# Kernel optimization log

Measured on AMD Instinct MI355X. Metric: run time of the kernel, lower is better.

Reference implementation:

```python
import jax, jax.numpy as jnp
import numpy as np

R = 8  # rnn_radius
C = 64  # channels


def _shift(x, dh, dw):
    # out[b, h, w, c] = x[b, h - dh, w - dw, c], zero padded (matches SAME conv with a single masked tap)
    B, H, W, Cc = x.shape
    x = jnp.pad(x, ((0, 0), (max(dh, 0), max(-dh, 0)), (max(dw, 0), max(-dw, 0)), (0, 0)))
    return x[:, max(-dh, 0):max(-dh, 0) + H, max(-dw, 0):max(-dw, 0) + W, :]


def _direction(x, W, dh, dw):
    # recurrent: t = relu(shift(t) @ W); acc = x + sum_t over R steps
    def step(carry, _):
        t, acc = carry
        t = jax.nn.relu(jnp.einsum('bhwc,cd->bhwd', _shift(t, dh, dw), W))
        return (t, acc + t), None
    (_, acc), _ = jax.lax.scan(step, (x, x), None, length=R)
    return acc


def setup_inputs() -> dict:
    key = jax.random.key(0)
    kx, kl, kr, ku, kd = jax.random.split(key, 5)
    x = jax.random.normal(kx, (8, 192, 192, C), dtype=jnp.float32)
    # masked kernels reduce to a single CxC channel-mix matrix per direction
    # (keras 'random_normal' initializer: stddev 0.05)
    W_left = jax.random.normal(kl, (C, C), dtype=jnp.float32) * 0.05
    W_right = jax.random.normal(kr, (C, C), dtype=jnp.float32) * 0.05
    W_up = jax.random.normal(ku, (C, C), dtype=jnp.float32) * 0.05
    W_down = jax.random.normal(kd, (C, C), dtype=jnp.float32) * 0.05
    return {"x": x, "W_left": W_left, "W_right": W_right, "W_up": W_up, "W_down": W_down}


def reference(x, W_left, W_right, W_up, W_down):
    # kernel_switch tap positions: left -> out[w]=in[w-1]; right -> out[w]=in[w+1];
    # up -> out[h]=in[h-1]; down -> out[h]=in[h+1]
    outs = [
        _direction(x, W_left, 0, 1),
        _direction(x, W_right, 0, -1),
        _direction(x, W_up, 1, 0),
        _direction(x, W_down, -1, 0),
    ]
    return jnp.concatenate(outs, axis=3)
```

## Files before the change

kernel.cpp:

```cpp
#include <hip/hip_runtime.h>
#include <hip/hip_bf16.h>


#define HD 192
#define CH 64
#define RSTEPS 8
#define TSTRIDE 72
#define SLOTS 193
#define STG_STRIDE 68

typedef __attribute__((ext_vector_type(8))) short short8v;
typedef __attribute__((ext_vector_type(4))) float float4v;

static __device__ __forceinline__ short f2bf_rne(float f) {
    unsigned u = __float_as_uint(f);
    u += 0x7FFFu + ((u >> 16) & 1u);
    return (short)(u >> 16);
}

__global__ __launch_bounds__(256) void spatial_rnn_kernel(
    const float* __restrict__ x,
    const float* __restrict__ Wl,
    const float* __restrict__ Wr,
    const float* __restrict__ Wu,
    const float* __restrict__ Wd,
    float* __restrict__ out)
{
    __shared__ __align__(16) short smem_s[2 * SLOTS * TSTRIDE];
    short* tb0 = smem_s;
    short* tb1 = smem_s + SLOTS * TSTRIDE;
    float* stg = (float*)smem_s;

    const int tid  = threadIdx.x;
    const int dir  = blockIdx.y;
    const int line = blockIdx.x;
    const int b    = line / HD;
    const int rc   = line - b * HD;

    const float* Wp = (dir == 0) ? Wl : (dir == 1) ? Wr : (dir == 2) ? Wu : Wd;

    int xbase, xstride, obase, ostride;
    if (dir == 0) {
        xbase   = (b * HD + rc) * HD * CH;
        xstride = CH;
        obase   = (b * HD + rc) * HD * 256;
        ostride = 256;
    } else if (dir == 1) {
        xbase   = ((b * HD + rc) * HD + (HD - 1)) * CH;
        xstride = -CH;
        obase   = ((b * HD + rc) * HD + (HD - 1)) * 256 + 64;
        ostride = -256;
    } else if (dir == 2) {
        xbase   = b * HD * HD * CH + rc * CH;
        xstride = HD * CH;
        obase   = b * HD * HD * 256 + rc * 256 + 128;
        ostride = HD * 256;
    } else {
        xbase   = ((b * HD + (HD - 1)) * HD + rc) * CH;
        xstride = -HD * CH;
        obase   = ((b * HD + (HD - 1)) * HD + rc) * 256 + 192;
        ostride = -HD * 256;
    }

    for (int q = tid; q < HD * 16; q += 256) {
        int p  = q >> 4;
        int c4 = (q & 15) << 2;
        const float4 v = *(const float4*)(x + xbase + p * xstride + c4);
        short4 s;
        s.x = f2bf_rne(v.x); s.y = f2bf_rne(v.y);
        s.z = f2bf_rne(v.z); s.w = f2bf_rne(v.w);
        *(short4*)(tb0 + (p + 1) * TSTRIDE + c4) = s;
    }
    if (tid < TSTRIDE) { tb0[tid] = 0; tb1[tid] = 0; }

    const int lane = tid & 63;
    const int wv   = tid >> 6;
    const int q4   = lane >> 4;
    const int l16  = lane & 15;

    short8v Af[2][4];
    #pragma unroll
    for (int kc = 0; kc < 2; ++kc)
        #pragma unroll
        for (int dt = 0; dt < 4; ++dt)
            #pragma unroll
            for (int j = 0; j < 8; ++j)
                Af[kc][dt][j] = f2bf_rne(Wp[(kc * 32 + q4 * 8 + j) * CH + dt * 16 + l16]);

    float4v acc[3][4];
    #pragma unroll
    for (int i = 0; i < 3; ++i)
        #pragma unroll
        for (int dt = 0; dt < 4; ++dt)
            acc[i][dt] = (float4v){0.f, 0.f, 0.f, 0.f};

    __syncthreads();

    for (int k = 0; k < RSTEPS; ++k) {
        const short* cur = (k & 1) ? tb1 : tb0;
        short*       nxt = (k & 1) ? tb0 : tb1;
        #pragma unroll
        for (int i = 0; i < 3; ++i) {
            const int pb   = (wv + i * 4) * 16;
            const int slot = pb + l16;
            short8v B0 = *(const short8v*)(cur + slot * TSTRIDE + q4 * 8);
            short8v B1 = *(const short8v*)(cur + slot * TSTRIDE + 32 + q4 * 8);
            #pragma unroll
            for (int dt = 0; dt < 4; ++dt) {
                float4v d = {0.f, 0.f, 0.f, 0.f};
                d = __builtin_amdgcn_mfma_f32_16x16x32_bf16(Af[0][dt], B0, d, 0, 0, 0);
                d = __builtin_amdgcn_mfma_f32_16x16x32_bf16(Af[1][dt], B1, d, 0, 0, 0);
                float v0 = fmaxf(d[0], 0.f);
                float v1 = fmaxf(d[1], 0.f);
                float v2 = fmaxf(d[2], 0.f);
                float v3 = fmaxf(d[3], 0.f);
                acc[i][dt][0] += v0; acc[i][dt][1] += v1;
                acc[i][dt][2] += v2; acc[i][dt][3] += v3;
                if (k < RSTEPS - 1) {
                    __hip_bfloat162 h01 = __float22bfloat162_rn(make_float2(v0, v1));
                    __hip_bfloat162 h23 = __float22bfloat162_rn(make_float2(v2, v3));
                    uint2 wpk;
                    __builtin_memcpy(&wpk.x, &h01, 4);
                    __builtin_memcpy(&wpk.y, &h23, 4);
                    *(uint2*)(nxt + (pb + l16 + 1) * TSTRIDE + dt * 16 + q4 * 4) = wpk;
                }
            }
        }
        __syncthreads();
    }

    #pragma unroll
    for (int i = 0; i < 3; ++i) {
        const int pb = (wv + i * 4) * 16;
        #pragma unroll
        for (int dt = 0; dt < 4; ++dt) {
            *(float4v*)(stg + (pb + l16) * STG_STRIDE + dt * 16 + q4 * 4) = acc[i][dt];
        }
    }
    __syncthreads();

    for (int q = tid; q < HD * 16; q += 256) {
        int p  = q >> 4;
        int c4 = (q & 15) << 2;
        const float4  xv = *(const float4*)(x + xbase + p * xstride + c4);
        const float4v sv = *(const float4v*)(stg + p * STG_STRIDE + c4);
        float4 o;
        o.x = xv.x + sv[0]; o.y = xv.y + sv[1];
        o.z = xv.z + sv[2]; o.w = xv.w + sv[3];
        *(float4*)(out + obase + p * ostride + c4) = o;
    }
}

extern "C" void kernel_launch(void* const* d_in, const int* in_sizes, int n_in,
                              void* d_out, int out_size, void* d_ws, size_t ws_size,
                              hipStream_t stream) {
    const float* x  = (const float*)d_in[0];
    const float* Wl = (const float*)d_in[1];
    const float* Wr = (const float*)d_in[2];
    const float* Wu = (const float*)d_in[3];
    const float* Wd = (const float*)d_in[4];
    float* outp = (float*)d_out;
    dim3 grid(8 * HD, 4);
    spatial_rnn_kernel<<<grid, 256, 0, stream>>>(x, Wl, Wr, Wu, Wd, outp);
}
```

Measured before the change: 518.7 us.

## Single-buffer LDS state, load x in MFMA layout, drop staging pass

Switches from double-buffered LDS to a single buffer: each step loads its B fragments into registers, syncs, then overwrites the buffer in place. x is now loaded directly in the MFMA output layout, which seeds the accumulator and the bf16 state in one pass. The epilogue writes the accumulators straight to global memory, removing the LDS staging step and the second read of x. Halving LDS use and adding a launch-bounds occupancy hint of 4 blocks should raise occupancy, at the cost of an extra barrier per step and less coalesced global accesses.

```diff
diff --git a/kernel.cpp b/kernel.cpp
--- a/kernel.cpp
+++ b/kernel.cpp
@@ -7,7 +7,6 @@
 #define RSTEPS 8
 #define TSTRIDE 72
 #define SLOTS 193
-#define STG_STRIDE 68
 
 typedef __attribute__((ext_vector_type(8))) short short8v;
 typedef __attribute__((ext_vector_type(4))) float float4v;
@@ -18,7 +17,7 @@
     return (short)(u >> 16);
 }
 
-__global__ __launch_bounds__(256) void spatial_rnn_kernel(
+__global__ __launch_bounds__(256, 4) void spatial_rnn_kernel(
     const float* __restrict__ x,
     const float* __restrict__ Wl,
     const float* __restrict__ Wr,
@@ -26,10 +25,7 @@
     const float* __restrict__ Wd,
     float* __restrict__ out)
 {
-    __shared__ __align__(16) short smem_s[2 * SLOTS * TSTRIDE];
-    short* tb0 = smem_s;
-    short* tb1 = smem_s + SLOTS * TSTRIDE;
-    float* stg = (float*)smem_s;
+    __shared__ __align__(16) short tb[SLOTS * TSTRIDE];
 
     const int tid  = threadIdx.x;
     const int dir  = blockIdx.y;
@@ -62,21 +58,29 @@
         ostride = -HD * 256;
     }
 
-    for (int q = tid; q < HD * 16; q += 256) {
-        int p  = q >> 4;
-        int c4 = (q & 15) << 2;
-        const float4 v = *(const float4*)(x + xbase + p * xstride + c4);
-        short4 s;
-        s.x = f2bf_rne(v.x); s.y = f2bf_rne(v.y);
-        s.z = f2bf_rne(v.z); s.w = f2bf_rne(v.w);
-        *(short4*)(tb0 + (p + 1) * TSTRIDE + c4) = s;
-    }
-    if (tid < TSTRIDE) { tb0[tid] = 0; tb1[tid] = 0; }
-
     const int lane = tid & 63;
     const int wv   = tid >> 6;
     const int q4   = lane >> 4;
     const int l16  = lane & 15;
+
+    if (tid < TSTRIDE) tb[tid] = 0;
+
+    float4v acc[3][4];
+    #pragma unroll
+    for (int i = 0; i < 3; ++i) {
+        const int p = (wv + i * 4) * 16 + l16;
+        #pragma unroll
+        for (int dt = 0; dt < 4; ++dt) {
+            const float4 v = *(const float4*)(x + xbase + p * xstride + dt * 16 + q4 * 4);
+            acc[i][dt] = (float4v){v.x, v.y, v.z, v.w};
+            __hip_bfloat162 h01 = __float22bfloat162_rn(make_float2(v.x, v.y));
+            __hip_bfloat162 h23 = __float22bfloat162_rn(make_float2(v.z, v.w));
+            uint2 wpk;
+            __builtin_memcpy(&wpk.x, &h01, 4);
+            __builtin_memcpy(&wpk.y, &h23, 4);
+            *(uint2*)(tb + (p + 1) * TSTRIDE + dt * 16 + q4 * 4) = wpk;
+        }
+    }
 
     short8v Af[2][4];
     #pragma unroll
@@ -87,29 +91,25 @@
             for (int j = 0; j < 8; ++j)
                 Af[kc][dt][j] = f2bf_rne(Wp[(kc * 32 + q4 * 8 + j) * CH + dt * 16 + l16]);
 
-    float4v acc[3][4];
-    #pragma unroll
-    for (int i = 0; i < 3; ++i)
-        #pragma unroll
-        for (int dt = 0; dt < 4; ++dt)
-            acc[i][dt] = (float4v){0.f, 0.f, 0.f, 0.f};
-
     __syncthreads();
 
     for (int k = 0; k < RSTEPS; ++k) {
-        const short* cur = (k & 1) ? tb1 : tb0;
-        short*       nxt = (k & 1) ? tb0 : tb1;
+        short8v B0[3], B1[3];
         #pragma unroll
         for (int i = 0; i < 3; ++i) {
-            const int pb   = (wv + i * 4) * 16;
-            const int slot = pb + l16;
-            short8v B0 = *(const short8v*)(cur + slot * TSTRIDE + q4 * 8);
-            short8v B1 = *(const short8v*)(cur + slot * TSTRIDE + 32 + q4 * 8);
+            const int slot = (wv + i * 4) * 16 + l16;
+            B0[i] = *(const short8v*)(tb + slot * TSTRIDE + q4 * 8);
+            B1[i] = *(const short8v*)(tb + slot * TSTRIDE + 32 + q4 * 8);
+        }
+        __syncthreads();
+        #pragma unroll
+        for (int i = 0; i < 3; ++i) {
+            const int pb = (wv + i * 4) * 16;
             #pragma unroll
             for (int dt = 0; dt < 4; ++dt) {
                 float4v d = {0.f, 0.f, 0.f, 0.f};
-                d = __builtin_amdgcn_mfma_f32_16x16x32_bf16(Af[0][dt], B0, d, 0, 0, 0);
-                d = __builtin_amdgcn_mfma_f32_16x16x32_bf16(Af[1][dt], B1, d, 0, 0, 0);
+                d = __builtin_amdgcn_mfma_f32_16x16x32_bf16(Af[0][dt], B0[i], d, 0, 0, 0);
+                d = __builtin_amdgcn_mfma_f32_16x16x32_bf16(Af[1][dt], B1[i], d, 0, 0, 0);
                 float v0 = fmaxf(d[0], 0.f);
                 float v1 = fmaxf(d[1], 0.f);
                 float v2 = fmaxf(d[2], 0.f);
@@ -122,32 +122,23 @@
                     uint2 wpk;
                     __builtin_memcpy(&wpk.x, &h01, 4);
                     __builtin_memcpy(&wpk.y, &h23, 4);
-                    *(uint2*)(nxt + (pb + l16 + 1) * TSTRIDE + dt * 16 + q4 * 4) = wpk;
+                    *(uint2*)(tb + (pb + l16 + 1) * TSTRIDE + dt * 16 + q4 * 4) = wpk;
                 }
             }
         }
-        __syncthreads();
+        if (k < RSTEPS - 1) __syncthreads();
     }
 
     #pragma unroll
     for (int i = 0; i < 3; ++i) {
-        const int pb = (wv + i * 4) * 16;
+        const int p = (wv + i * 4) * 16 + l16;
         #pragma unroll
         for (int dt = 0; dt < 4; ++dt) {
-            *(float4v*)(stg + (pb + l16) * STG_STRIDE + dt * 16 + q4 * 4) = acc[i][dt];
+            float4 o;
+            o.x = acc[i][dt][0]; o.y = acc[i][dt][1];
+            o.z = acc[i][dt][2]; o.w = acc[i][dt][3];
+            *(float4*)(out + obase + p * ostride + dt * 16 + q4 * 4) = o;
         }
-    }
-    __syncthreads();
-
-    for (int q = tid; q < HD * 16; q += 256) {
-        int p  = q >> 4;
-        int c4 = (q & 15) << 2;
-        const float4  xv = *(const float4*)(x + xbase + p * xstride + c4);
-        const float4v sv = *(const float4v*)(stg + p * STG_STRIDE + c4);
-        float4 o;
-        o.x = xv.x + sv[0]; o.y = xv.y + sv[1];
-        o.z = xv.z + sv[2]; o.w = xv.w + sv[3];
-        *(float4*)(out + obase + p * ostride + c4) = o;
     }
 }
 
```

Measured after the change: 417.6 us. -19.5%, faster.
